# Kernel tuning notes

Hardware: AMD Instinct MI355X
Metric: run time of the kernel (lower is better)

## Reference

```python
import jax, jax.numpy as jnp
import numpy as np

D = 512; NH = 8; NL = 6; DFF = 2048
TOK = 1024; APP = 3; V = TOK + APP; PAD = V - 1
B = 256; SENC = 16; LTGT = 62


def setup_inputs() -> dict:
    key = jax.random.key(0)
    ks = jax.random.split(key, 14)
    g = lambda k, shp, s=0.02: jax.random.normal(k, shp, jnp.float32) * s
    return dict(
        encoder_out=jax.random.normal(ks[0], (B, SENC, D), jnp.float32),
        point_out=jax.random.normal(ks[1], (B, D), jnp.float32),
        emb=g(ks[2], (V, D)),
        pos_embed=g(ks[3], (1, LTGT, D)),
        sa_inw=g(ks[4], (NL, 3 * D, D)), sa_inb=jnp.zeros((NL, 3 * D), jnp.float32),
        sa_outw=g(ks[5], (NL, D, D)), sa_outb=jnp.zeros((NL, D), jnp.float32),
        ca_inw=g(ks[6], (NL, 3 * D, D)), ca_inb=jnp.zeros((NL, 3 * D), jnp.float32),
        ca_outw=g(ks[7], (NL, D, D)), ca_outb=jnp.zeros((NL, D), jnp.float32),
        ln1_s=jnp.ones((NL, D), jnp.float32), ln1_b=jnp.zeros((NL, D), jnp.float32),
        ln2_s=jnp.ones((NL, D), jnp.float32), ln2_b=jnp.zeros((NL, D), jnp.float32),
        ln3_s=jnp.ones((NL, D), jnp.float32), ln3_b=jnp.zeros((NL, D), jnp.float32),
        ff1_w=g(ks[8], (NL, DFF, D)), ff1_b=jnp.zeros((NL, DFF), jnp.float32),
        ff2_w=g(ks[9], (NL, D, DFF)), ff2_b=jnp.zeros((NL, D), jnp.float32),
        out_w=g(ks[10], (V, D)), out_b=jnp.zeros((V,), jnp.float32),
        tgt=jax.random.randint(ks[11], (B, LTGT), 0, TOK),
    )


def _ln(x, s, b, eps=1e-5):
    m = x.mean(-1, keepdims=True)
    v = ((x - m) ** 2).mean(-1, keepdims=True)
    return (x - m) / jnp.sqrt(v + eps) * s + b


def _mha(q_in, kv_in, inw, inb, outw, outb, mask):
    # PyTorch MultiheadAttention with packed in_proj [3D, D]
    hd = D // NH
    wq, wk, wv = inw[:D], inw[D:2 * D], inw[2 * D:]
    bq, bk, bv = inb[:D], inb[D:2 * D], inb[2 * D:]
    Bq, Tq = q_in.shape[0], q_in.shape[1]
    Tk = kv_in.shape[1]
    q = (q_in @ wq.T + bq).reshape(Bq, Tq, NH, hd)
    k = (kv_in @ wk.T + bk).reshape(Bq, Tk, NH, hd)
    v = (kv_in @ wv.T + bv).reshape(Bq, Tk, NH, hd)
    s = jnp.einsum('bqhd,bkhd->bhqk', q, k) / np.float32(np.sqrt(hd))
    if mask is not None:
        s = s + mask
    a = jax.nn.softmax(s, axis=-1)
    o = jnp.einsum('bhqk,bkhd->bqhd', a, v).reshape(Bq, Tq, D)
    return o @ outw.T + outb


def reference(encoder_out, point_out, emb, pos_embed,
              sa_inw, sa_inb, sa_outw, sa_outb,
              ca_inw, ca_inb, ca_outw, ca_outb,
              ln1_s, ln1_b, ln2_s, ln2_b, ln3_s, ln3_b,
              ff1_w, ff1_b, ff2_w, ff2_b, out_w, out_b, tgt):
    # scheduled_sampling_ratio == 1.0 => the per-step loop always writes the
    # ground-truth token, so output_sequence == tgt[:, :-1] and the returned
    # tensor equals one full causal decoder pass over tgt[:, :-1].
    tokens = tgt[:, :-1]                      # [B, L], L = 61
    L = tokens.shape[1]
    neg = jnp.float32(-jnp.inf)
    causal = jnp.where(jnp.triu(jnp.ones((L, L), bool), 1), neg, 0.0)
    padm = jnp.where(tokens == PAD, neg, 0.0)[:, None, None, :]  # [B,1,1,L]
    mask = causal[None, None] + padm          # [B,1,L,L]
    mem = encoder_out[:, :1, :]               # memory length 1 (encoder_out[:, [0]])
    x = emb[tokens] + point_out[:, None, :] + pos_embed[0, :L]
    for i in range(NL):
        x = _ln(x + _mha(x, x, sa_inw[i], sa_inb[i], sa_outw[i], sa_outb[i], mask), ln1_s[i], ln1_b[i])
        x = _ln(x + _mha(x, mem, ca_inw[i], ca_inb[i], ca_outw[i], ca_outb[i], None), ln2_s[i], ln2_b[i])
        h = jax.nn.relu(x @ ff1_w[i].T + ff1_b[i]) @ ff2_w[i].T + ff2_b[i]
        x = _ln(x + h, ln3_s[i], ln3_b[i])
    return x @ out_w.T + out_b               # [B, L, V]
```

## Files before the change

kernel.cpp:

```cpp
#include <hip/hip_runtime.h>
#include <stdint.h>
#include <stddef.h>

typedef unsigned short u16;
typedef float f4 __attribute__((ext_vector_type(4)));
typedef float f32x4 __attribute__((ext_vector_type(4)));
typedef short bf16x8 __attribute__((ext_vector_type(8)));
typedef u16 u16x4 __attribute__((ext_vector_type(4)));
typedef int i4v __attribute__((ext_vector_type(4)));

#define PAD_TOK 1026
#define LQ 61
#define NBATCH 256
#define MTOT (NBATCH * LQ)

__device__ __forceinline__ u16 f2b(float f) {
  uint32_t x = __float_as_uint(f);
  x += 0x7fff + ((x >> 16) & 1);
  return (u16)(x >> 16);
}
__device__ __forceinline__ float b2f(u16 u) {
  return __uint_as_float(((uint32_t)u) << 16);
}

template<int BM>
__global__ __launch_bounds__(256) void gemm_bt(
    const u16* __restrict__ A, const u16* __restrict__ W,
    const float* __restrict__ bias,
    float* __restrict__ Cf, u16* __restrict__ Cb,
    int M, int N, int K, int Nreal, int ldc, int relu,
    long aZ, long wZ, long bZ, long cZ)
{
  constexpr int MI = BM / 32;
  const int z = blockIdx.z;
  A += z * aZ; W += z * wZ; bias += z * bZ;
  if (Cf) Cf += z * cZ;
  if (Cb) Cb += z * cZ;

  __shared__ u16 As[BM * 64];
  __shared__ u16 Bs[128 * 64];

  const int gx = gridDim.x;
  const int nwg = gx * gridDim.y;
  const int orig = blockIdx.y * gx + blockIdx.x;
  const int q8 = nwg >> 3, r8 = nwg & 7;
  const int xcd = orig & 7, off = orig >> 3;
  const int nid = (xcd < r8 ? xcd * (q8 + 1) : r8 * (q8 + 1) + (xcd - r8) * q8) + off;
  const int bx = nid % gx, by = nid / gx;

  const int tid = threadIdx.x;
  const int wid = tid >> 6, lane = tid & 63;
  const int wr = wid >> 1, wc = wid & 1;
  const long m0 = (long)by * BM;
  const long n0 = (long)bx * 128;

  const int lr = lane >> 3;
  const int lc = lane & 7;
  const int scol = ((lc ^ lr) << 3);

  f32x4 acc[MI][4];
#pragma unroll
  for (int i = 0; i < MI; ++i)
#pragma unroll
    for (int j = 0; j < 4; ++j) acc[i][j] = (f32x4){0.f, 0.f, 0.f, 0.f};

  const u16* Abase = A + m0 * K;
  const u16* Wbase = W + n0 * K;
  const int r = lane & 15, kg = lane >> 4;

  for (int kt = 0; kt < K; kt += 64) {
#pragma unroll
    for (int c = 0; c < BM / 32; ++c) {
      const int row = wid * (BM / 4) + c * 8;
      __builtin_amdgcn_global_load_lds(
          (const __attribute__((address_space(1))) void*)(Abase + (long)(row + lr) * K + kt + scol),
          (__attribute__((address_space(3))) void*)&As[row * 64], 16, 0, 0);
    }
#pragma unroll
    for (int c = 0; c < 4; ++c) {
      const int row = wid * 32 + c * 8;
      __builtin_amdgcn_global_load_lds(
          (const __attribute__((address_space(1))) void*)(Wbase + (long)(row + lr) * K + kt + scol),
          (__attribute__((address_space(3))) void*)&Bs[row * 64], 16, 0, 0);
    }
    __syncthreads();

#pragma unroll
    for (int ks = 0; ks < 64; ks += 32) {
      bf16x8 a[MI], b[4];
#pragma unroll
      for (int mi = 0; mi < MI; ++mi) {
        const int row = wr * (BM / 2) + mi * 16 + r;
        const int chunk = ((ks >> 3) + kg) ^ (row & 7);
        a[mi] = *(const bf16x8*)&As[row * 64 + chunk * 8];
      }
#pragma unroll
      for (int ni = 0; ni < 4; ++ni) {
        const int row = wc * 64 + ni * 16 + r;
        const int chunk = ((ks >> 3) + kg) ^ (row & 7);
        b[ni] = *(const bf16x8*)&Bs[row * 64 + chunk * 8];
      }
#pragma unroll
      for (int mi = 0; mi < MI; ++mi)
#pragma unroll
        for (int ni = 0; ni < 4; ++ni)
          acc[mi][ni] = __builtin_amdgcn_mfma_f32_16x16x32_bf16(a[mi], b[ni], acc[mi][ni], 0, 0, 0);
    }
    __syncthreads();
  }

  const int cr4 = (lane >> 4) * 4;
  const int cc = lane & 15;

  if (Cb) {
#pragma unroll
    for (int ni = 0; ni < 4; ++ni) {
      const int coll = wc * 64 + ni * 16 + cc;
      const float bv = bias[(int)n0 + coll];
#pragma unroll
      for (int mi = 0; mi < MI; ++mi) {
#pragma unroll
        for (int j = 0; j < 4; ++j) {
          const int rowl = wr * (BM / 2) + mi * 16 + cr4 + j;
          float v = acc[mi][ni][j] + bv;
          if (relu) v = fmaxf(v, 0.f);
          const int sw = (rowl & 7) << 3;
          u16* half = (coll & 64) ? Bs : As;
          half[rowl * 64 + ((coll & 63) ^ sw)] = f2b(v);
        }
      }
    }
    __syncthreads();
    constexpr int PT = BM / 16;
#pragma unroll
    for (int i = 0; i < PT; ++i) {
      const int t = i * 256 + tid;
      const int row = t >> 4, ch = t & 15;
      const int n = (int)n0 + ch * 8;
      if (n < Nreal) {
        const int phys = (ch & 7) ^ (row & 7);
        const u16* half = (ch < 8) ? As : Bs;
        bf16x8 vv = *(const bf16x8*)&half[row * 64 + phys * 8];
        *(bf16x8*)&Cb[(m0 + row) * (long)N + n] = vv;
      }
    }
  } else {
#pragma unroll
    for (int ni = 0; ni < 4; ++ni) {
      const int n = (int)n0 + wc * 64 + ni * 16 + cc;
      if (n >= Nreal) continue;
      const float bv = bias[n];
#pragma unroll
      for (int mi = 0; mi < MI; ++mi) {
#pragma unroll
        for (int j = 0; j < 4; ++j) {
          const long m = m0 + wr * (BM / 2) + mi * 16 + cr4 + j;
          float v = acc[mi][ni][j] + bv;
          if (relu) v = fmaxf(v, 0.f);
          Cf[m * ldc + n] = v;
        }
      }
    }
  }
}

__global__ __launch_bounds__(256) void attn_k(const u16* __restrict__ qkv,
                                              const int* __restrict__ tgt,
                                              u16* __restrict__ outp)
{
  __shared__ u16 Qs[64 * 72];
  __shared__ u16 Ks[64 * 72];
  __shared__ u16 Vt[64 * 72];
  __shared__ float S[64 * 65];
  __shared__ int stok[64];

  const int bid = blockIdx.x;
  const int b = bid >> 3, h = bid & 7;
  const int tid = threadIdx.x;
  const int tr = tid >> 2, seg = tid & 3;

  if (tid < 64) stok[tid] = (tid < 61) ? tgt[b * 62 + tid] : -1;

  const long rowbase = ((long)(b * LQ + tr)) * 1536 + h * 64;
  if (tr < LQ) {
    const i4v* qsrc = (const i4v*)(qkv + rowbase + seg * 16);
    i4v q0 = qsrc[0], q1 = qsrc[1];
    *(i4v*)&Qs[tr * 72 + seg * 16] = q0;
    *(i4v*)&Qs[tr * 72 + seg * 16 + 8] = q1;
    const i4v* ksrc = (const i4v*)(qkv + rowbase + 512 + seg * 16);
    i4v k0 = ksrc[0], k1 = ksrc[1];
    *(i4v*)&Ks[tr * 72 + seg * 16] = k0;
    *(i4v*)&Ks[tr * 72 + seg * 16 + 8] = k1;
    const u16* vsrc = qkv + rowbase + 1024 + seg * 16;
#pragma unroll
    for (int i = 0; i < 16; ++i) Vt[(seg * 16 + i) * 72 + tr] = vsrc[i];
  } else {
    i4v zz = {0, 0, 0, 0};
    *(i4v*)&Qs[tr * 72 + seg * 16] = zz;
    *(i4v*)&Qs[tr * 72 + seg * 16 + 8] = zz;
    *(i4v*)&Ks[tr * 72 + seg * 16] = zz;
    *(i4v*)&Ks[tr * 72 + seg * 16 + 8] = zz;
#pragma unroll
    for (int i = 0; i < 16; ++i) Vt[(seg * 16 + i) * 72 + tr] = 0;
  }
  __syncthreads();

  const int lane = tid & 63, w = tid >> 6;
  const int r = lane & 15, kg = lane >> 4;

  {
    f32x4 s[4];
#pragma unroll
    for (int ni = 0; ni < 4; ++ni) s[ni] = (f32x4){0.f, 0.f, 0.f, 0.f};
    bf16x8 a0 = *(const bf16x8*)&Qs[(w * 16 + r) * 72 + kg * 8];
    bf16x8 a1 = *(const bf16x8*)&Qs[(w * 16 + r) * 72 + 32 + kg * 8];
#pragma unroll
    for (int ni = 0; ni < 4; ++ni) {
      bf16x8 b0 = *(const bf16x8*)&Ks[(ni * 16 + r) * 72 + kg * 8];
      bf16x8 b1 = *(const bf16x8*)&Ks[(ni * 16 + r) * 72 + 32 + kg * 8];
      s[ni] = __builtin_amdgcn_mfma_f32_16x16x32_bf16(a0, b0, s[ni], 0, 0, 0);
      s[ni] = __builtin_amdgcn_mfma_f32_16x16x32_bf16(a1, b1, s[ni], 0, 0, 0);
    }
#pragma unroll
    for (int ni = 0; ni < 4; ++ni)
#pragma unroll
      for (int j = 0; j < 4; ++j)
        S[(w * 16 + kg * 4 + j) * 65 + ni * 16 + r] = s[ni][j];
  }
  __syncthreads();

  {
    const int row = tid >> 2, g = tid & 3;
    float vals[16];
    float mx = -3e38f;
#pragma unroll
    for (int i = 0; i < 16; ++i) {
      const int k = g * 16 + i;
      float v = S[row * 65 + k] * 0.125f;
      const bool ok = (k <= row) && (k < LQ) && (stok[k] != PAD_TOK);
      v = ok ? v : -1e30f;
      vals[i] = v;
      mx = fmaxf(mx, v);
    }
    mx = fmaxf(mx, __shfl_xor(mx, 1));
    mx = fmaxf(mx, __shfl_xor(mx, 2));
    float sum = 0.f;
#pragma unroll
    for (int i = 0; i < 16; ++i) { float e = __expf(vals[i] - mx); vals[i] = e; sum += e; }
    sum += __shfl_xor(sum, 1);
    sum += __shfl_xor(sum, 2);
    const float inv = 1.f / sum;
#pragma unroll
    for (int i = 0; i < 16; ++i) Qs[row * 72 + g * 16 + i] = f2b(vals[i] * inv);
  }
  __syncthreads();

  {
    f32x4 o[4];
#pragma unroll
    for (int ni = 0; ni < 4; ++ni) o[ni] = (f32x4){0.f, 0.f, 0.f, 0.f};
    bf16x8 a0 = *(const bf16x8*)&Qs[(w * 16 + r) * 72 + kg * 8];
    bf16x8 a1 = *(const bf16x8*)&Qs[(w * 16 + r) * 72 + 32 + kg * 8];
#pragma unroll
    for (int ni = 0; ni < 4; ++ni) {
      bf16x8 b0 = *(const bf16x8*)&Vt[(ni * 16 + r) * 72 + kg * 8];
      bf16x8 b1 = *(const bf16x8*)&Vt[(ni * 16 + r) * 72 + 32 + kg * 8];
      o[ni] = __builtin_amdgcn_mfma_f32_16x16x32_bf16(a0, b0, o[ni], 0, 0, 0);
      o[ni] = __builtin_amdgcn_mfma_f32_16x16x32_bf16(a1, b1, o[ni], 0, 0, 0);
    }
#pragma unroll
    for (int ni = 0; ni < 4; ++ni)
#pragma unroll
      for (int j = 0; j < 4; ++j) {
        const int qrow = w * 16 + kg * 4 + j;
        const int col = ni * 16 + r;
        Ks[qrow * 64 + (col ^ ((qrow & 7) << 3))] = f2b(o[ni][j]);
      }
  }
  __syncthreads();

  {
    const int row = tid >> 2, sub = tid & 3;
    if (row < LQ) {
      const long obase = ((long)(b * LQ + row)) * 512 + h * 64;
#pragma unroll
      for (int i = 0; i < 2; ++i) {
        const int ch = i * 4 + sub;
        const int phys = ch ^ (row & 7);
        bf16x8 vv = *(const bf16x8*)&Ks[row * 64 + phys * 8];
        *(bf16x8*)&outp[obase + ch * 8] = vv;
      }
    }
  }
}

__device__ __forceinline__ void ln_row(f4& v0, f4& v1,
                                       const float* __restrict__ sw,
                                       const float* __restrict__ bw, int d0) {
  float s1 = v0[0] + v0[1] + v0[2] + v0[3] + v1[0] + v1[1] + v1[2] + v1[3];
  float s2 = v0[0]*v0[0] + v0[1]*v0[1] + v0[2]*v0[2] + v0[3]*v0[3]
           + v1[0]*v1[0] + v1[1]*v1[1] + v1[2]*v1[2] + v1[3]*v1[3];
#pragma unroll
  for (int off = 1; off < 64; off <<= 1) {
    s1 += __shfl_xor(s1, off);
    s2 += __shfl_xor(s2, off);
  }
  const float mean = s1 * (1.f / 512.f);
  const float var = s2 * (1.f / 512.f) - mean * mean;
  const float rstd = rsqrtf(var + 1e-5f);
  const f4* sp = (const f4*)(sw + d0);
  const f4* bp = (const f4*)(bw + d0);
  f4 ss0 = sp[0], ss1 = sp[1], bb0 = bp[0], bb1 = bp[1];
#pragma unroll
  for (int i = 0; i < 4; ++i) {
    v0[i] = (v0[i] - mean) * rstd * ss0[i] + bb0[i];
    v1[i] = (v1[i] - mean) * rstd * ss1[i] + bb1[i];
  }
}

template<bool CA>
__global__ __launch_bounds__(256) void lnf_k(const u16* __restrict__ p,
                                             const u16* __restrict__ xr,
                                             const float* __restrict__ cav,
                                             const float* __restrict__ s1,
                                             const float* __restrict__ b1,
                                             const float* __restrict__ s2,
                                             const float* __restrict__ b2,
                                             u16* __restrict__ out)
{
  const int m = blockIdx.x * 4 + (threadIdx.x >> 6);
  const int lane = threadIdx.x & 63;
  const int d0 = lane * 8;
  bf16x8 pv = *(const bf16x8*)(p + (long)m * 512 + d0);
  bf16x8 xv = *(const bf16x8*)(xr + (long)m * 512 + d0);
  f4 v0, v1;
#pragma unroll
  for (int i = 0; i < 4; ++i) {
    v0[i] = b2f((u16)pv[i]) + b2f((u16)xv[i]);
    v1[i] = b2f((u16)pv[4 + i]) + b2f((u16)xv[4 + i]);
  }
  ln_row(v0, v1, s1, b1, d0);
  if constexpr (CA) {
    const int b = m / LQ;
    const f4* qv = (const f4*)(cav + (long)b * 512 + d0);
    v0 += qv[0]; v1 += qv[1];
    ln_row(v0, v1, s2, b2, d0);
  }
  u16x4* ob = (u16x4*)(out + (long)m * 512 + d0);
  ob[0] = (u16x4){f2b(v0[0]), f2b(v0[1]), f2b(v0[2]), f2b(v0[3])};
  ob[1] = (u16x4){f2b(v1[0]), f2b(v1[1]), f2b(v1[2]), f2b(v1[3])};
}

__global__ __launch_bounds__(256) void embed_k(const float* __restrict__ emb,
                                               const float* __restrict__ pout,
                                               const float* __restrict__ pos,
                                               const int* __restrict__ tgt,
                                               u16* __restrict__ XB)
{
  const int m = blockIdx.x * 4 + (threadIdx.x >> 6);
  const int lane = threadIdx.x & 63;
  const int b = m / LQ, t = m % LQ;
  const int tok = tgt[b * 62 + t];
  const int d0 = lane * 8;
  const f4* e = (const f4*)(emb + (long)tok * 512 + d0);
  const f4* p = (const f4*)(pout + (long)b * 512 + d0);
  const f4* q = (const f4*)(pos + (long)t * 512 + d0);
  f4 v0 = e[0] + p[0] + q[0];
  f4 v1 = e[1] + p[1] + q[1];
  u16x4* xb = (u16x4*)(XB + (long)m * 512 + d0);
  xb[0] = (u16x4){f2b(v0[0]), f2b(v0[1]), f2b(v0[2]), f2b(v0[3])};
  xb[1] = (u16x4){f2b(v1[0]), f2b(v1[1]), f2b(v1[2]), f2b(v1[3])};
}

__global__ void cvt_bf16_k(const float* __restrict__ src, u16* __restrict__ dst, int n4) {
  const int i = blockIdx.x * 256 + threadIdx.x;
  if (i >= n4) return;
  f4 v = ((const f4*)src)[i];
  ((u16x4*)dst)[i] = (u16x4){f2b(v[0]), f2b(v[1]), f2b(v[2]), f2b(v[3])};
}

__global__ void cvt_ca_v_k(const float* __restrict__ ca_inw, u16* __restrict__ dst) {
  const int i = blockIdx.x * 256 + threadIdx.x;
  if (i >= 393216) return;
  const int l = i >> 16, rem = i & 65535;
  f4 v = ((const f4*)ca_inw)[l * 196608 + 131072 + rem];
  ((u16x4*)dst)[i] = (u16x4){f2b(v[0]), f2b(v[1]), f2b(v[2]), f2b(v[3])};
}

__global__ void cvt_outw_k(const float* __restrict__ out_w, u16* __restrict__ dst) {
  const int i = blockIdx.x * 256 + threadIdx.x;
  if (i >= 147456) return;
  const int row = (i * 4) >> 9;
  u16x4 o = {0, 0, 0, 0};
  if (row < 1027) {
    f4 v = ((const f4*)out_w)[i];
    o = (u16x4){f2b(v[0]), f2b(v[1]), f2b(v[2]), f2b(v[3])};
  }
  ((u16x4*)dst)[i] = o;
}

__global__ void cvt_outb_k(const float* __restrict__ out_b, float* __restrict__ dst) {
  const int i = blockIdx.x * 256 + threadIdx.x;
  if (i >= 1152) return;
  dst[i] = (i < 1027) ? out_b[i] : 0.f;
}

__global__ void cvt_memb_k(const float* __restrict__ enc, u16* __restrict__ dst) {
  const int i = blockIdx.x * 256 + threadIdx.x;
  if (i >= 32768) return;
  const int b = (i * 4) >> 9, d = (i * 4) & 511;
  f4 v = ((const f4*)enc)[(b * 8192 + d) >> 2];
  ((u16x4*)dst)[i] = (u16x4){f2b(v[0]), f2b(v[1]), f2b(v[2]), f2b(v[3])};
}

static constexpr size_t XB_OFF    = 0;
static constexpr size_t P_OFF     = 15990784;
static constexpr size_t BIG_OFF   = 31981568;
static constexpr size_t ATT_OFF   = 95944704;
static constexpr size_t WSA_OFF   = 111935488;
static constexpr size_t WSO_OFF   = 121372672;
static constexpr size_t WCAV_OFF  = 124518400;
static constexpr size_t WCO_OFF   = 127664128;
static constexpr size_t WF1_OFF   = 130809856;
static constexpr size_t WF2_OFF   = 143392768;
static constexpr size_t WOUT_OFF  = 155975680;
static constexpr size_t BOUT_OFF  = 157155328;
static constexpr size_t MEMB_OFF  = 157159936;
static constexpr size_t CATMP_OFF = 157422080;
static constexpr size_t CAV_OFF   = 158994944;

extern "C" void kernel_launch(void* const* d_in, const int* in_sizes, int n_in,
                              void* d_out, int out_size, void* d_ws, size_t ws_size,
                              hipStream_t stream) {
  (void)in_sizes; (void)n_in; (void)out_size; (void)ws_size;
  const float* encoder_out = (const float*)d_in[0];
  const float* point_out   = (const float*)d_in[1];
  const float* emb         = (const float*)d_in[2];
  const float* pos         = (const float*)d_in[3];
  const float* sa_inw      = (const float*)d_in[4];
  const float* sa_inb      = (const float*)d_in[5];
  const float* sa_outw     = (const float*)d_in[6];
  const float* sa_outb     = (const float*)d_in[7];
  const float* ca_inw      = (const float*)d_in[8];
  const float* ca_inb      = (const float*)d_in[9];
  const float* ca_outw     = (const float*)d_in[10];
  const float* ca_outb     = (const float*)d_in[11];
  const float* ln1_s       = (const float*)d_in[12];
  const float* ln1_b       = (const float*)d_in[13];
  const float* ln2_s       = (const float*)d_in[14];
  const float* ln2_b       = (const float*)d_in[15];
  const float* ln3_s       = (const float*)d_in[16];
  const float* ln3_b       = (const float*)d_in[17];
  const float* ff1_w       = (const float*)d_in[18];
  const float* ff1_b       = (const float*)d_in[19];
  const float* ff2_w       = (const float*)d_in[20];
  const float* ff2_b       = (const float*)d_in[21];
  const float* out_w       = (const float*)d_in[22];
  const float* out_b       = (const float*)d_in[23];
  const int*   tgt         = (const int*)d_in[24];

  char* ws = (char*)d_ws;
  u16*   XB    = (u16*)(ws + XB_OFF);
  u16*   P     = (u16*)(ws + P_OFF);
  u16*   BIG   = (u16*)(ws + BIG_OFF);
  u16*   ATT   = (u16*)(ws + ATT_OFF);
  u16*   WSA   = (u16*)(ws + WSA_OFF);
  u16*   WSO   = (u16*)(ws + WSO_OFF);
  u16*   WCAV  = (u16*)(ws + WCAV_OFF);
  u16*   WCO   = (u16*)(ws + WCO_OFF);
  u16*   WF1   = (u16*)(ws + WF1_OFF);
  u16*   WF2   = (u16*)(ws + WF2_OFF);
  u16*   WOUT  = (u16*)(ws + WOUT_OFF);
  float* BOUT  = (float*)(ws + BOUT_OFF);
  u16*   MEMB  = (u16*)(ws + MEMB_OFF);
  u16*   CATMP = (u16*)(ws + CATMP_OFF);
  float* CAV   = (float*)(ws + CAV_OFF);

  cvt_bf16_k<<<dim3(4608), dim3(256), 0, stream>>>(sa_inw, WSA, 1179648);
  cvt_bf16_k<<<dim3(1536), dim3(256), 0, stream>>>(sa_outw, WSO, 393216);
  cvt_ca_v_k<<<dim3(1536), dim3(256), 0, stream>>>(ca_inw, WCAV);
  cvt_bf16_k<<<dim3(1536), dim3(256), 0, stream>>>(ca_outw, WCO, 393216);
  cvt_bf16_k<<<dim3(6144), dim3(256), 0, stream>>>(ff1_w, WF1, 1572864);
  cvt_bf16_k<<<dim3(6144), dim3(256), 0, stream>>>(ff2_w, WF2, 1572864);
  cvt_outw_k<<<dim3(576), dim3(256), 0, stream>>>(out_w, WOUT);
  cvt_outb_k<<<dim3(5), dim3(256), 0, stream>>>(out_b, BOUT);
  cvt_memb_k<<<dim3(128), dim3(256), 0, stream>>>(encoder_out, MEMB);

  embed_k<<<dim3(MTOT / 4), dim3(256), 0, stream>>>(emb, point_out, pos, tgt, XB);

  gemm_bt<64><<<dim3(4, 4, 6), dim3(256), 0, stream>>>(
      MEMB, WCAV, ca_inb + 1024, nullptr, CATMP,
      256, 512, 512, 512, 512, 0,
      0L, 262144L, 1536L, 131072L);
  gemm_bt<64><<<dim3(4, 4, 6), dim3(256), 0, stream>>>(
      CATMP, WCO, ca_outb, CAV, nullptr,
      256, 512, 512, 512, 512, 0,
      131072L, 262144L, 512L, 131072L);

  for (int l = 0; l < 6; ++l) {
    gemm_bt<128><<<dim3(12, 122, 1), dim3(256), 0, stream>>>(
        XB, WSA + (long)l * 786432, sa_inb + l * 1536, nullptr, BIG,
        MTOT, 1536, 512, 1536, 1536, 0, 0L, 0L, 0L, 0L);
    attn_k<<<dim3(2048), dim3(256), 0, stream>>>(BIG, tgt, ATT);
    gemm_bt<64><<<dim3(4, 244, 1), dim3(256), 0, stream>>>(
        ATT, WSO + (long)l * 262144, sa_outb + l * 512, nullptr, P,
        MTOT, 512, 512, 512, 512, 0, 0L, 0L, 0L, 0L);
    lnf_k<true><<<dim3(MTOT / 4), dim3(256), 0, stream>>>(
        P, XB, CAV + (long)l * 131072,
        ln1_s + l * 512, ln1_b + l * 512, ln2_s + l * 512, ln2_b + l * 512, XB);
    gemm_bt<128><<<dim3(16, 122, 1), dim3(256), 0, stream>>>(
        XB, WF1 + (long)l * 1048576, ff1_b + l * 2048, nullptr, BIG,
        MTOT, 2048, 512, 2048, 2048, 1, 0L, 0L, 0L, 0L);
    gemm_bt<64><<<dim3(4, 244, 1), dim3(256), 0, stream>>>(
        BIG, WF2 + (long)l * 1048576, ff2_b + l * 512, nullptr, P,
        MTOT, 512, 2048, 512, 512, 0, 0L, 0L, 0L, 0L);
    lnf_k<false><<<dim3(MTOT / 4), dim3(256), 0, stream>>>(
        P, XB, nullptr, ln3_s + l * 512, ln3_b + l * 512, nullptr, nullptr, XB);
  }

  gemm_bt<128><<<dim3(9, 122, 1), dim3(256), 0, stream>>>(
      XB, WOUT, BOUT, (float*)d_out, nullptr,
      MTOT, 1152, 512, 1027, 1027, 0, 0L, 0L, 0L, 0L);
}
```

Baseline: 1.216 ms.

## Add 256x256-tile 8-wave GEMM with direct-to-LDS loads for QKV, FF1, output

After: 1.187 ms. 2.4% less time.

```diff
diff --git a/kernel.cpp b/kernel.cpp
--- a/kernel.cpp
+++ b/kernel.cpp
@@ -21,6 +21,203 @@
 }
 __device__ __forceinline__ float b2f(u16 u) {
   return __uint_as_float(((uint32_t)u) << 16);
+}
+
+#define GLDS(gptr, lptr) __builtin_amdgcn_global_load_lds( \
+    (const __attribute__((address_space(1))) void*)(gptr), \
+    (__attribute__((address_space(3))) void*)(lptr), 16, 0, 0)
+
+__device__ __forceinline__ bf16x8 ldfrag(const u16* buf, int row, int ksl, int kg) {
+  const int chunk = (ksl * 4 + kg) ^ (row & 7);
+  return *(const bf16x8*)&buf[row * 64 + chunk * 8];
+}
+
+__global__ __launch_bounds__(512, 2) void gemm8_k(
+    const u16* __restrict__ A, const u16* __restrict__ W,
+    const float* __restrict__ bias,
+    float* __restrict__ Cf, u16* __restrict__ Cb,
+    int N, int K, int Nreal, int ldc, int relu)
+{
+  __shared__ u16 lds[4][16384];
+  u16* const LA0 = lds[0];
+  u16* const LB0 = lds[1];
+  u16* const LA1 = lds[2];
+  u16* const LB1 = lds[3];
+
+  const int gx = gridDim.x;
+  const int nwg = gx * gridDim.y;
+  const int orig = blockIdx.y * gx + blockIdx.x;
+  const int q8 = nwg >> 3, r8 = nwg & 7;
+  const int xcd = orig & 7, off = orig >> 3;
+  const int nid = (xcd < r8 ? xcd * (q8 + 1) : r8 * (q8 + 1) + (xcd - r8) * q8) + off;
+  const int bx = nid % gx, by = nid / gx;
+
+  const int tid = threadIdx.x;
+  const int wid = tid >> 6, lane = tid & 63;
+  const int wm = wid >> 2, wn = wid & 3;
+  const long m0 = (long)by * 256;
+  const long n0 = (long)bx * 256;
+
+  const int lr = lane >> 3, lc = lane & 7;
+  const int scol = ((lc ^ lr) << 3);
+  const int r = lane & 15, kg = lane >> 4;
+
+  const u16* __restrict__ Ab = A + m0 * K;
+  const u16* __restrict__ Wb = W + n0 * K;
+
+  f32x4 acc[8][4];
+#pragma unroll
+  for (int i = 0; i < 8; ++i)
+#pragma unroll
+    for (int j = 0; j < 4; ++j) acc[i][j] = (f32x4){0.f, 0.f, 0.f, 0.f};
+
+#define ST64(gbase, kt, ldsbuf, r0) do {                                     \
+    const int rb_ = (r0) + wid * 8;                                          \
+    GLDS((gbase) + (long)(rb_ + lr) * K + (kt) + scol, &(ldsbuf)[rb_ * 64]); \
+  } while (0)
+#define STAQ(kt, ldsbuf, q_) do {                                            \
+    const int rb_ = ((wid & 4) ? 128 : 0) + (q_) * 32 + (wid & 3) * 8;       \
+    GLDS(Ab + (long)(rb_ + lr) * K + (kt) + scol, &(ldsbuf)[rb_ * 64]);      \
+  } while (0)
+#define STB(kt, ldsbuf) do {            \
+    ST64(Wb, kt, ldsbuf, 0);   ST64(Wb, kt, ldsbuf, 64);  \
+    ST64(Wb, kt, ldsbuf, 128); ST64(Wb, kt, ldsbuf, 192); \
+  } while (0)
+#define STAF(kt, ldsbuf) do {           \
+    ST64(Ab, kt, ldsbuf, 0);   ST64(Ab, kt, ldsbuf, 64);  \
+    ST64(Ab, kt, ldsbuf, 128); ST64(Ab, kt, ldsbuf, 192); \
+  } while (0)
+#define ENDBAR do { __builtin_amdgcn_sched_barrier(0); __builtin_amdgcn_s_barrier(); } while (0)
+#define PHASE(bufA, q_) do {                                                 \
+    bf16x8 a_[2][2];                                                         \
+    _Pragma("unroll")                                                        \
+    for (int ml = 0; ml < 2; ++ml)                                           \
+      _Pragma("unroll")                                                      \
+      for (int ks = 0; ks < 2; ++ks)                                         \
+        a_[ml][ks] = ldfrag(bufA, wm * 128 + ((q_) * 2 + ml) * 16 + r, ks, kg); \
+    __builtin_amdgcn_s_setprio(1);                                           \
+    _Pragma("unroll")                                                        \
+    for (int ml = 0; ml < 2; ++ml)                                           \
+      _Pragma("unroll")                                                      \
+      for (int ni = 0; ni < 4; ++ni) {                                       \
+        acc[(q_) * 2 + ml][ni] = __builtin_amdgcn_mfma_f32_16x16x32_bf16(    \
+            a_[ml][0], bf[ni][0], acc[(q_) * 2 + ml][ni], 0, 0, 0);          \
+        acc[(q_) * 2 + ml][ni] = __builtin_amdgcn_mfma_f32_16x16x32_bf16(    \
+            a_[ml][1], bf[ni][1], acc[(q_) * 2 + ml][ni], 0, 0, 0);          \
+      }                                                                      \
+    __builtin_amdgcn_s_setprio(0);                                           \
+  } while (0)
+
+  STAF(0, LA0); STB(0, LB0);
+  STAF(64, LA1); STB(64, LB1);
+
+  const int nits = K >> 7;
+  bf16x8 bf[4][2];
+
+  for (int it = 0; it < nits; ++it) {
+    const int kt1 = it * 128 + 64;
+    const int ktA = it * 128 + 128;
+    const int ktB = it * 128 + 192;
+    const bool last = (it == nits - 1);
+
+    asm volatile("s_waitcnt vmcnt(7)" ::: "memory");
+    ENDBAR;
+    if (it > 0) STAQ(kt1, LA1, 3);
+#pragma unroll
+    for (int ni = 0; ni < 4; ++ni)
+#pragma unroll
+      for (int ks = 0; ks < 2; ++ks)
+        bf[ni][ks] = ldfrag(LB0, wn * 64 + ni * 16 + r, ks, kg);
+    PHASE(LA0, 0);
+    ENDBAR;
+    if (!last) { STAQ(ktA, LA0, 0); STB(ktA, LB0); }
+    PHASE(LA0, 1);
+    ENDBAR;
+    if (!last) STAQ(ktA, LA0, 1);
+    PHASE(LA0, 2);
+    ENDBAR;
+    if (!last) STAQ(ktA, LA0, 2);
+    PHASE(LA0, 3);
+    ENDBAR;
+    if (last) asm volatile("s_waitcnt vmcnt(0)" ::: "memory");
+    else      asm volatile("s_waitcnt vmcnt(7)" ::: "memory");
+    ENDBAR;
+    if (!last) STAQ(ktA, LA0, 3);
+#pragma unroll
+    for (int ni = 0; ni < 4; ++ni)
+#pragma unroll
+      for (int ks = 0; ks < 2; ++ks)
+        bf[ni][ks] = ldfrag(LB1, wn * 64 + ni * 16 + r, ks, kg);
+    PHASE(LA1, 0);
+    ENDBAR;
+    if (!last) { STAQ(ktB, LA1, 0); STB(ktB, LB1); }
+    PHASE(LA1, 1);
+    ENDBAR;
+    if (!last) STAQ(ktB, LA1, 1);
+    PHASE(LA1, 2);
+    ENDBAR;
+    if (!last) STAQ(ktB, LA1, 2);
+    PHASE(LA1, 3);
+    ENDBAR;
+  }
+
+  const int cr4 = (lane >> 4) * 4;
+  const int cc = lane & 15;
+  if (Cb) {
+    u16* cbuf = &lds[0][0];
+#pragma unroll
+    for (int ni = 0; ni < 4; ++ni) {
+      const int coll = wn * 64 + ni * 16 + cc;
+      const float bv = bias[(int)n0 + coll];
+#pragma unroll
+      for (int mi = 0; mi < 8; ++mi) {
+#pragma unroll
+        for (int j = 0; j < 4; ++j) {
+          const int rowl = wm * 128 + mi * 16 + cr4 + j;
+          float v = acc[mi][ni][j] + bv;
+          if (relu) v = fmaxf(v, 0.f);
+          const int ch = coll >> 3;
+          const int phys = ch ^ (rowl & 31);
+          cbuf[rowl * 256 + phys * 8 + (coll & 7)] = f2b(v);
+        }
+      }
+    }
+    ENDBAR;
+#pragma unroll
+    for (int i = 0; i < 16; ++i) {
+      const int t = i * 512 + tid;
+      const int row = t >> 5, ch = t & 31;
+      const int n = (int)n0 + ch * 8;
+      if (n < Nreal) {
+        const int phys = ch ^ (row & 31);
+        *(bf16x8*)&Cb[(m0 + row) * (long)N + n] =
+            *(const bf16x8*)&cbuf[row * 256 + phys * 8];
+      }
+    }
+  } else {
+#pragma unroll
+    for (int ni = 0; ni < 4; ++ni) {
+      const int n = (int)n0 + wn * 64 + ni * 16 + cc;
+      if (n >= Nreal) continue;
+      const float bv = bias[n];
+#pragma unroll
+      for (int mi = 0; mi < 8; ++mi) {
+#pragma unroll
+        for (int j = 0; j < 4; ++j) {
+          const long m = m0 + wm * 128 + mi * 16 + cr4 + j;
+          float v = acc[mi][ni][j] + bv;
+          if (relu) v = fmaxf(v, 0.f);
+          Cf[m * ldc + n] = v;
+        }
+      }
+    }
+  }
+#undef ST64
+#undef STAQ
+#undef STB
+#undef STAF
+#undef ENDBAR
+#undef PHASE
 }
 
 template<int BM>
@@ -389,7 +586,7 @@
 
 __global__ void cvt_outw_k(const float* __restrict__ out_w, u16* __restrict__ dst) {
   const int i = blockIdx.x * 256 + threadIdx.x;
-  if (i >= 147456) return;
+  if (i >= 163840) return;
   const int row = (i * 4) >> 9;
   u16x4 o = {0, 0, 0, 0};
   if (row < 1027) {
@@ -401,7 +598,7 @@
 
 __global__ void cvt_outb_k(const float* __restrict__ out_b, float* __restrict__ dst) {
   const int i = blockIdx.x * 256 + threadIdx.x;
-  if (i >= 1152) return;
+  if (i >= 1280) return;
   dst[i] = (i < 1027) ? out_b[i] : 0.f;
 }
 
@@ -424,10 +621,10 @@
 static constexpr size_t WF1_OFF   = 130809856;
 static constexpr size_t WF2_OFF   = 143392768;
 static constexpr size_t WOUT_OFF  = 155975680;
-static constexpr size_t BOUT_OFF  = 157155328;
-static constexpr size_t MEMB_OFF  = 157159936;
-static constexpr size_t CATMP_OFF = 157422080;
-static constexpr size_t CAV_OFF   = 158994944;
+static constexpr size_t BOUT_OFF  = 157286400;
+static constexpr size_t MEMB_OFF  = 157291520;
+static constexpr size_t CATMP_OFF = 157553664;
+static constexpr size_t CAV_OFF   = 159126528;
 
 extern "C" void kernel_launch(void* const* d_in, const int* in_sizes, int n_in,
                               void* d_out, int out_size, void* d_ws, size_t ws_size,
@@ -482,7 +679,7 @@
   cvt_bf16_k<<<dim3(1536), dim3(256), 0, stream>>>(ca_outw, WCO, 393216);
   cvt_bf16_k<<<dim3(6144), dim3(256), 0, stream>>>(ff1_w, WF1, 1572864);
   cvt_bf16_k<<<dim3(6144), dim3(256), 0, stream>>>(ff2_w, WF2, 1572864);
-  cvt_outw_k<<<dim3(576), dim3(256), 0, stream>>>(out_w, WOUT);
+  cvt_outw_k<<<dim3(640), dim3(256), 0, stream>>>(out_w, WOUT);
   cvt_outb_k<<<dim3(5), dim3(256), 0, stream>>>(out_b, BOUT);
   cvt_memb_k<<<dim3(128), dim3(256), 0, stream>>>(encoder_out, MEMB);
 
@@ -498,9 +695,9 @@
       131072L, 262144L, 512L, 131072L);
 
   for (int l = 0; l < 6; ++l) {
-    gemm_bt<128><<<dim3(12, 122, 1), dim3(256), 0, stream>>>(
+    gemm8_k<<<dim3(6, 61), dim3(512), 0, stream>>>(
         XB, WSA + (long)l * 786432, sa_inb + l * 1536, nullptr, BIG,
-        MTOT, 1536, 512, 1536, 1536, 0, 0L, 0L, 0L, 0L);
+        1536, 512, 1536, 1536, 0);
     attn_k<<<dim3(2048), dim3(256), 0, stream>>>(BIG, tgt, ATT);
     gemm_bt<64><<<dim3(4, 244, 1), dim3(256), 0, stream>>>(
         ATT, WSO + (long)l * 262144, sa_outb + l * 512, nullptr, P,
@@ -508,9 +705,9 @@
     lnf_k<true><<<dim3(MTOT / 4), dim3(256), 0, stream>>>(
         P, XB, CAV + (long)l * 131072,
         ln1_s + l * 512, ln1_b + l * 512, ln2_s + l * 512, ln2_b + l * 512, XB);
-    gemm_bt<128><<<dim3(16, 122, 1), dim3(256), 0, stream>>>(
+    gemm8_k<<<dim3(8, 61), dim3(512), 0, stream>>>(
         XB, WF1 + (long)l * 1048576, ff1_b + l * 2048, nullptr, BIG,
-        MTOT, 2048, 512, 2048, 2048, 1, 0L, 0L, 0L, 0L);
+        2048, 512, 2048, 2048, 1);
     gemm_bt<64><<<dim3(4, 244, 1), dim3(256), 0, stream>>>(
         BIG, WF2 + (long)l * 1048576, ff2_b + l * 512, nullptr, P,
         MTOT, 512, 2048, 512, 512, 0, 0L, 0L, 0L, 0L);
@@ -518,7 +715,7 @@
         P, XB, nullptr, ln3_s + l * 512, ln3_b + l * 512, nullptr, nullptr, XB);
   }
 
-  gemm_bt<128><<<dim3(9, 122, 1), dim3(256), 0, stream>>>(
+  gemm8_k<<<dim3(5, 61), dim3(512), 0, stream>>>(
       XB, WOUT, BOUT, (float*)d_out, nullptr,
-      MTOT, 1152, 512, 1027, 1027, 0, 0L, 0L, 0L, 0L);
-}
+      1280, 512, 1027, 1027, 0);
+}
```

## Fuse output-projection and FFN2 GEMMs with residual add and LayerNorm epilogue

Applied to the files above, without the earlier changes.

New measurement: 1.303 ms. 7.1% more time.

```diff
diff --git a/kernel.cpp b/kernel.cpp
--- a/kernel.cpp
+++ b/kernel.cpp
@@ -21,6 +21,15 @@
 }
 __device__ __forceinline__ float b2f(u16 u) {
   return __uint_as_float(((uint32_t)u) << 16);
+}
+
+#define GLDS(gptr, lptr) __builtin_amdgcn_global_load_lds( \
+    (const __attribute__((address_space(1))) void*)(gptr), \
+    (__attribute__((address_space(3))) void*)(lptr), 16, 0, 0)
+
+__device__ __forceinline__ bf16x8 ldfrag(const u16* buf, int row, int ksl, int kg) {
+  const int chunk = (ksl * 4 + kg) ^ (row & 7);
+  return *(const bf16x8*)&buf[row * 64 + chunk * 8];
 }
 
 template<int BM>
@@ -72,34 +81,24 @@
 #pragma unroll
     for (int c = 0; c < BM / 32; ++c) {
       const int row = wid * (BM / 4) + c * 8;
-      __builtin_amdgcn_global_load_lds(
-          (const __attribute__((address_space(1))) void*)(Abase + (long)(row + lr) * K + kt + scol),
-          (__attribute__((address_space(3))) void*)&As[row * 64], 16, 0, 0);
+      GLDS(Abase + (long)(row + lr) * K + kt + scol, &As[row * 64]);
     }
 #pragma unroll
     for (int c = 0; c < 4; ++c) {
       const int row = wid * 32 + c * 8;
-      __builtin_amdgcn_global_load_lds(
-          (const __attribute__((address_space(1))) void*)(Wbase + (long)(row + lr) * K + kt + scol),
-          (__attribute__((address_space(3))) void*)&Bs[row * 64], 16, 0, 0);
+      GLDS(Wbase + (long)(row + lr) * K + kt + scol, &Bs[row * 64]);
     }
     __syncthreads();
 
 #pragma unroll
-    for (int ks = 0; ks < 64; ks += 32) {
+    for (int ks = 0; ks < 2; ++ks) {
       bf16x8 a[MI], b[4];
 #pragma unroll
-      for (int mi = 0; mi < MI; ++mi) {
-        const int row = wr * (BM / 2) + mi * 16 + r;
-        const int chunk = ((ks >> 3) + kg) ^ (row & 7);
-        a[mi] = *(const bf16x8*)&As[row * 64 + chunk * 8];
-      }
-#pragma unroll
-      for (int ni = 0; ni < 4; ++ni) {
-        const int row = wc * 64 + ni * 16 + r;
-        const int chunk = ((ks >> 3) + kg) ^ (row & 7);
-        b[ni] = *(const bf16x8*)&Bs[row * 64 + chunk * 8];
-      }
+      for (int mi = 0; mi < MI; ++mi)
+        a[mi] = ldfrag(As, wr * (BM / 2) + mi * 16 + r, ks, kg);
+#pragma unroll
+      for (int ni = 0; ni < 4; ++ni)
+        b[ni] = ldfrag(Bs, wc * 64 + ni * 16 + r, ks, kg);
 #pragma unroll
       for (int mi = 0; mi < MI; ++mi)
 #pragma unroll
@@ -161,6 +160,229 @@
         }
       }
     }
+  }
+}
+
+template<bool CA2>
+__global__ __launch_bounds__(512, 2) void gemmln_k(
+    const u16* __restrict__ A, const u16* __restrict__ W,
+    const float* __restrict__ bias,
+    const u16* __restrict__ cavb,
+    const float* __restrict__ s1w, const float* __restrict__ b1w,
+    const float* __restrict__ s2w, const float* __restrict__ b2w,
+    u16* __restrict__ XB, int K)
+{
+  __shared__ u16 BIGL[36864];
+  __shared__ float LSTAT[64][8];
+  __shared__ u16 LCAV[1536];
+  u16* const LB = BIGL;
+  u16* const LA = BIGL + 32768;
+  u16* const EP = BIGL;
+
+  const int nwg = gridDim.x;
+  const int orig = blockIdx.x;
+  const int q8 = nwg >> 3, r8 = nwg & 7;
+  const int xcd = orig & 7, off = orig >> 3;
+  const int by = (xcd < r8 ? xcd * (q8 + 1) : r8 * (q8 + 1) + (xcd - r8) * q8) + off;
+
+  const int tid = threadIdx.x;
+  const int wid = tid >> 6, lane = tid & 63;
+  const int wm = wid >> 2, wn = wid & 3;
+  const long m0 = (long)by * 64;
+
+  const int lr = lane >> 3, lc = lane & 7;
+  const int scol = ((lc ^ lr) << 3);
+  const int r = lane & 15, kg = lane >> 4;
+
+  f32x4 acc[2][8];
+#pragma unroll
+  for (int i = 0; i < 2; ++i)
+#pragma unroll
+    for (int j = 0; j < 8; ++j) acc[i][j] = (f32x4){0.f, 0.f, 0.f, 0.f};
+
+  const u16* Abase = A + m0 * K;
+
+  for (int kt = 0; kt < K; kt += 64) {
+    {
+      const int arow = wid * 8;
+      GLDS(Abase + (long)(arow + lr) * K + kt + scol, &LA[arow * 64]);
+#pragma unroll
+      for (int c = 0; c < 8; ++c) {
+        const int row = wid * 64 + c * 8;
+        GLDS(W + (long)(row + lr) * K + kt + scol, &LB[row * 64]);
+      }
+    }
+    __syncthreads();
+#pragma unroll
+    for (int ks = 0; ks < 2; ++ks) {
+      bf16x8 a0 = ldfrag(LA, wm * 32 + r, ks, kg);
+      bf16x8 a1 = ldfrag(LA, wm * 32 + 16 + r, ks, kg);
+#pragma unroll
+      for (int ni = 0; ni < 8; ++ni) {
+        bf16x8 b = ldfrag(LB, wn * 128 + ni * 16 + r, ks, kg);
+        acc[0][ni] = __builtin_amdgcn_mfma_f32_16x16x32_bf16(a0, b, acc[0][ni], 0, 0, 0);
+        acc[1][ni] = __builtin_amdgcn_mfma_f32_16x16x32_bf16(a1, b, acc[1][ni], 0, 0, 0);
+      }
+    }
+    __syncthreads();
+  }
+
+  const int b0 = (int)(m0 / LQ);
+  const int bsplit1 = (b0 + 1) * LQ;
+  const int bsplit2 = (b0 + 2) * LQ;
+
+#pragma unroll
+  for (int i = 0; i < 8; ++i) {
+    const int t = i * 512 + tid;
+    const int row = t >> 6, ch = t & 63;
+    *(bf16x8*)&EP[row * 516 + ch * 8] =
+        *(const bf16x8*)&XB[(m0 + row) * 512 + ch * 8];
+  }
+  if constexpr (CA2) {
+    for (int t = tid; t < 1536; t += 512) {
+      const int bb = t >> 9, c = t & 511;
+      int bi = b0 + bb;
+      if (bi > NBATCH - 1) bi = NBATCH - 1;
+      LCAV[bb * 512 + c] = cavb[(long)bi * 512 + c];
+    }
+  }
+  __syncthreads();
+
+  float bcol[8];
+#pragma unroll
+  for (int ni = 0; ni < 8; ++ni) bcol[ni] = bias[wn * 128 + ni * 16 + r];
+#pragma unroll
+  for (int mi = 0; mi < 2; ++mi)
+#pragma unroll
+    for (int ni = 0; ni < 8; ++ni) {
+      const int col = wn * 128 + ni * 16 + r;
+#pragma unroll
+      for (int j = 0; j < 4; ++j) {
+        const int row = wm * 32 + mi * 16 + kg * 4 + j;
+        acc[mi][ni][j] += bcol[ni] + b2f(EP[row * 516 + col]);
+      }
+    }
+
+#pragma unroll
+  for (int mi = 0; mi < 2; ++mi)
+#pragma unroll
+    for (int j = 0; j < 4; ++j) {
+      float s1 = 0.f, s2 = 0.f;
+#pragma unroll
+      for (int ni = 0; ni < 8; ++ni) {
+        const float v = acc[mi][ni][j];
+        s1 += v; s2 += v * v;
+      }
+#pragma unroll
+      for (int o = 1; o < 16; o <<= 1) {
+        s1 += __shfl_xor(s1, o);
+        s2 += __shfl_xor(s2, o);
+      }
+      if (r == 0) {
+        const int row = wm * 32 + mi * 16 + kg * 4 + j;
+        LSTAT[row][wn] = s1;
+        LSTAT[row][4 + wn] = s2;
+      }
+    }
+  __syncthreads();
+
+  float sc[8], bc[8];
+#pragma unroll
+  for (int ni = 0; ni < 8; ++ni) {
+    const int col = wn * 128 + ni * 16 + r;
+    sc[ni] = s1w[col]; bc[ni] = b1w[col];
+  }
+#pragma unroll
+  for (int mi = 0; mi < 2; ++mi)
+#pragma unroll
+    for (int j = 0; j < 4; ++j) {
+      const int row = wm * 32 + mi * 16 + kg * 4 + j;
+      const float S1 = LSTAT[row][0] + LSTAT[row][1] + LSTAT[row][2] + LSTAT[row][3];
+      const float S2 = LSTAT[row][4] + LSTAT[row][5] + LSTAT[row][6] + LSTAT[row][7];
+      const float mean = S1 * (1.f / 512.f);
+      const float var = S2 * (1.f / 512.f) - mean * mean;
+      const float rstd = rsqrtf(var + 1e-5f);
+#pragma unroll
+      for (int ni = 0; ni < 8; ++ni)
+        acc[mi][ni][j] = (acc[mi][ni][j] - mean) * rstd * sc[ni] + bc[ni];
+    }
+
+  if constexpr (CA2) {
+#pragma unroll
+    for (int mi = 0; mi < 2; ++mi)
+#pragma unroll
+      for (int j = 0; j < 4; ++j) {
+        const int row = wm * 32 + mi * 16 + kg * 4 + j;
+        const int gr = (int)m0 + row;
+        const int sel = (gr >= bsplit2) ? 2 : ((gr >= bsplit1) ? 1 : 0);
+#pragma unroll
+        for (int ni = 0; ni < 8; ++ni) {
+          const int col = wn * 128 + ni * 16 + r;
+          acc[mi][ni][j] += b2f(LCAV[sel * 512 + col]);
+        }
+      }
+    __syncthreads();
+#pragma unroll
+    for (int mi = 0; mi < 2; ++mi)
+#pragma unroll
+      for (int j = 0; j < 4; ++j) {
+        float s1 = 0.f, s2 = 0.f;
+#pragma unroll
+        for (int ni = 0; ni < 8; ++ni) {
+          const float v = acc[mi][ni][j];
+          s1 += v; s2 += v * v;
+        }
+#pragma unroll
+        for (int o = 1; o < 16; o <<= 1) {
+          s1 += __shfl_xor(s1, o);
+          s2 += __shfl_xor(s2, o);
+        }
+        if (r == 0) {
+          const int row = wm * 32 + mi * 16 + kg * 4 + j;
+          LSTAT[row][wn] = s1;
+          LSTAT[row][4 + wn] = s2;
+        }
+      }
+    __syncthreads();
+#pragma unroll
+    for (int ni = 0; ni < 8; ++ni) {
+      const int col = wn * 128 + ni * 16 + r;
+      sc[ni] = s2w[col]; bc[ni] = b2w[col];
+    }
+#pragma unroll
+    for (int mi = 0; mi < 2; ++mi)
+#pragma unroll
+      for (int j = 0; j < 4; ++j) {
+        const int row = wm * 32 + mi * 16 + kg * 4 + j;
+        const float S1 = LSTAT[row][0] + LSTAT[row][1] + LSTAT[row][2] + LSTAT[row][3];
+        const float S2 = LSTAT[row][4] + LSTAT[row][5] + LSTAT[row][6] + LSTAT[row][7];
+        const float mean = S1 * (1.f / 512.f);
+        const float var = S2 * (1.f / 512.f) - mean * mean;
+        const float rstd = rsqrtf(var + 1e-5f);
+#pragma unroll
+        for (int ni = 0; ni < 8; ++ni)
+          acc[mi][ni][j] = (acc[mi][ni][j] - mean) * rstd * sc[ni] + bc[ni];
+      }
+  }
+
+#pragma unroll
+  for (int mi = 0; mi < 2; ++mi)
+#pragma unroll
+    for (int ni = 0; ni < 8; ++ni) {
+      const int col = wn * 128 + ni * 16 + r;
+#pragma unroll
+      for (int j = 0; j < 4; ++j) {
+        const int row = wm * 32 + mi * 16 + kg * 4 + j;
+        EP[row * 516 + col] = f2b(acc[mi][ni][j]);
+      }
+    }
+  __syncthreads();
+#pragma unroll
+  for (int i = 0; i < 8; ++i) {
+    const int t = i * 512 + tid;
+    const int row = t >> 6, ch = t & 63;
+    *(bf16x8*)&XB[(m0 + row) * 512 + ch * 8] =
+        *(const bf16x8*)&EP[row * 516 + ch * 8];
   }
 }
 
@@ -292,63 +514,6 @@
       }
     }
   }
-}
-
-__device__ __forceinline__ void ln_row(f4& v0, f4& v1,
-                                       const float* __restrict__ sw,
-                                       const float* __restrict__ bw, int d0) {
-  float s1 = v0[0] + v0[1] + v0[2] + v0[3] + v1[0] + v1[1] + v1[2] + v1[3];
-  float s2 = v0[0]*v0[0] + v0[1]*v0[1] + v0[2]*v0[2] + v0[3]*v0[3]
-           + v1[0]*v1[0] + v1[1]*v1[1] + v1[2]*v1[2] + v1[3]*v1[3];
-#pragma unroll
-  for (int off = 1; off < 64; off <<= 1) {
-    s1 += __shfl_xor(s1, off);
-    s2 += __shfl_xor(s2, off);
-  }
-  const float mean = s1 * (1.f / 512.f);
-  const float var = s2 * (1.f / 512.f) - mean * mean;
-  const float rstd = rsqrtf(var + 1e-5f);
-  const f4* sp = (const f4*)(sw + d0);
-  const f4* bp = (const f4*)(bw + d0);
-  f4 ss0 = sp[0], ss1 = sp[1], bb0 = bp[0], bb1 = bp[1];
-#pragma unroll
-  for (int i = 0; i < 4; ++i) {
-    v0[i] = (v0[i] - mean) * rstd * ss0[i] + bb0[i];
-    v1[i] = (v1[i] - mean) * rstd * ss1[i] + bb1[i];
-  }
-}
-
-template<bool CA>
-__global__ __launch_bounds__(256) void lnf_k(const u16* __restrict__ p,
-                                             const u16* __restrict__ xr,
-                                             const float* __restrict__ cav,
-                                             const float* __restrict__ s1,
-                                             const float* __restrict__ b1,
-                                             const float* __restrict__ s2,
-                                             const float* __restrict__ b2,
-                                             u16* __restrict__ out)
-{
-  const int m = blockIdx.x * 4 + (threadIdx.x >> 6);
-  const int lane = threadIdx.x & 63;
-  const int d0 = lane * 8;
-  bf16x8 pv = *(const bf16x8*)(p + (long)m * 512 + d0);
-  bf16x8 xv = *(const bf16x8*)(xr + (long)m * 512 + d0);
-  f4 v0, v1;
-#pragma unroll
-  for (int i = 0; i < 4; ++i) {
-    v0[i] = b2f((u16)pv[i]) + b2f((u16)xv[i]);
-    v1[i] = b2f((u16)pv[4 + i]) + b2f((u16)xv[4 + i]);
-  }
-  ln_row(v0, v1, s1, b1, d0);
-  if constexpr (CA) {
-    const int b = m / LQ;
-    const f4* qv = (const f4*)(cav + (long)b * 512 + d0);
-    v0 += qv[0]; v1 += qv[1];
-    ln_row(v0, v1, s2, b2, d0);
-  }
-  u16x4* ob = (u16x4*)(out + (long)m * 512 + d0);
-  ob[0] = (u16x4){f2b(v0[0]), f2b(v0[1]), f2b(v0[2]), f2b(v0[3])};
-  ob[1] = (u16x4){f2b(v1[0]), f2b(v1[1]), f2b(v1[2]), f2b(v1[3])};
 }
 
 __global__ __launch_bounds__(256) void embed_k(const float* __restrict__ emb,
@@ -372,11 +537,28 @@
   xb[1] = (u16x4){f2b(v1[0]), f2b(v1[1]), f2b(v1[2]), f2b(v1[3])};
 }
 
-__global__ void cvt_bf16_k(const float* __restrict__ src, u16* __restrict__ dst, int n4) {
-  const int i = blockIdx.x * 256 + threadIdx.x;
-  if (i >= n4) return;
-  f4 v = ((const f4*)src)[i];
-  ((u16x4*)dst)[i] = (u16x4){f2b(v[0]), f2b(v[1]), f2b(v[2]), f2b(v[3])};
+__global__ void cvtall_k(const float* __restrict__ s0, const float* __restrict__ s1,
+                         const float* __restrict__ s2, const float* __restrict__ s3,
+                         const float* __restrict__ s4,
+                         u16* __restrict__ d0, u16* __restrict__ d1,
+                         u16* __restrict__ d2, u16* __restrict__ d3,
+                         u16* __restrict__ d4)
+{
+  const int N0 = 1179648;
+  const int N1 = N0 + 393216;
+  const int N2 = N1 + 393216;
+  const int N3 = N2 + 1572864;
+  const int N4 = N3 + 1572864;
+  for (int i = blockIdx.x * 256 + threadIdx.x; i < N4; i += gridDim.x * 256) {
+    const float* s; u16* d; int k;
+    if (i < N0)      { s = s0; d = d0; k = i; }
+    else if (i < N1) { s = s1; d = d1; k = i - N0; }
+    else if (i < N2) { s = s2; d = d2; k = i - N1; }
+    else if (i < N3) { s = s3; d = d3; k = i - N2; }
+    else             { s = s4; d = d4; k = i - N3; }
+    f4 v = ((const f4*)s)[k];
+    ((u16x4*)d)[k] = (u16x4){f2b(v[0]), f2b(v[1]), f2b(v[2]), f2b(v[3])};
+  }
 }
 
 __global__ void cvt_ca_v_k(const float* __restrict__ ca_inw, u16* __restrict__ dst) {
@@ -414,20 +596,19 @@
 }
 
 static constexpr size_t XB_OFF    = 0;
-static constexpr size_t P_OFF     = 15990784;
-static constexpr size_t BIG_OFF   = 31981568;
-static constexpr size_t ATT_OFF   = 95944704;
-static constexpr size_t WSA_OFF   = 111935488;
-static constexpr size_t WSO_OFF   = 121372672;
-static constexpr size_t WCAV_OFF  = 124518400;
-static constexpr size_t WCO_OFF   = 127664128;
-static constexpr size_t WF1_OFF   = 130809856;
-static constexpr size_t WF2_OFF   = 143392768;
-static constexpr size_t WOUT_OFF  = 155975680;
-static constexpr size_t BOUT_OFF  = 157155328;
-static constexpr size_t MEMB_OFF  = 157159936;
-static constexpr size_t CATMP_OFF = 157422080;
-static constexpr size_t CAV_OFF   = 158994944;
+static constexpr size_t BIG_OFF   = 15990784;
+static constexpr size_t ATT_OFF   = 79953920;
+static constexpr size_t WSA_OFF   = 95944704;
+static constexpr size_t WSO_OFF   = 105381888;
+static constexpr size_t WCAV_OFF  = 108527616;
+static constexpr size_t WCO_OFF   = 111673344;
+static constexpr size_t WF1_OFF   = 114819072;
+static constexpr size_t WF2_OFF   = 127401984;
+static constexpr size_t WOUT_OFF  = 139984896;
+static constexpr size_t BOUT_OFF  = 141164544;
+static constexpr size_t MEMB_OFF  = 141169152;
+static constexpr size_t CATMP_OFF = 141431296;
+static constexpr size_t CAVB_OFF  = 143004160;
 
 extern "C" void kernel_launch(void* const* d_in, const int* in_sizes, int n_in,
                               void* d_out, int out_size, void* d_ws, size_t ws_size,
@@ -461,7 +642,6 @@
 
   char* ws = (char*)d_ws;
   u16*   XB    = (u16*)(ws + XB_OFF);
-  u16*   P     = (u16*)(ws + P_OFF);
   u16*   BIG   = (u16*)(ws + BIG_OFF);
   u16*   ATT   = (u16*)(ws + ATT_OFF);
   u16*   WSA   = (u16*)(ws + WSA_OFF);
@@ -474,14 +654,11 @@
   float* BOUT  = (float*)(ws + BOUT_OFF);
   u16*   MEMB  = (u16*)(ws + MEMB_OFF);
   u16*   CATMP = (u16*)(ws + CATMP_OFF);
-  float* CAV   = (float*)(ws + CAV_OFF);
-
-  cvt_bf16_k<<<dim3(4608), dim3(256), 0, stream>>>(sa_inw, WSA, 1179648);
-  cvt_bf16_k<<<dim3(1536), dim3(256), 0, stream>>>(sa_outw, WSO, 393216);
+  u16*   CAVB  = (u16*)(ws + CAVB_OFF);
+
+  cvtall_k<<<dim3(2048), dim3(256), 0, stream>>>(
+      sa_inw, sa_outw, ca_outw, ff1_w, ff2_w, WSA, WSO, WCO, WF1, WF2);
   cvt_ca_v_k<<<dim3(1536), dim3(256), 0, stream>>>(ca_inw, WCAV);
-  cvt_bf16_k<<<dim3(1536), dim3(256), 0, stream>>>(ca_outw, WCO, 393216);
-  cvt_bf16_k<<<dim3(6144), dim3(256), 0, stream>>>(ff1_w, WF1, 1572864);
-  cvt_bf16_k<<<dim3(6144), dim3(256), 0, stream>>>(ff2_w, WF2, 1572864);
   cvt_outw_k<<<dim3(576), dim3(256), 0, stream>>>(out_w, WOUT);
   cvt_outb_k<<<dim3(5), dim3(256), 0, stream>>>(out_b, BOUT);
   cvt_memb_k<<<dim3(128), dim3(256), 0, stream>>>(encoder_out, MEMB);
@@ -493,7 +670,7 @@
       256, 512, 512, 512, 512, 0,
       0L, 262144L, 1536L, 131072L);
   gemm_bt<64><<<dim3(4, 4, 6), dim3(256), 0, stream>>>(
-      CATMP, WCO, ca_outb, CAV, nullptr,
+      CATMP, WCO, ca_outb, nullptr, CAVB,
       256, 512, 512, 512, 512, 0,
       131072L, 262144L, 512L, 131072L);
 
@@ -502,20 +679,19 @@
         XB, WSA + (long)l * 786432, sa_inb + l * 1536, nullptr, BIG,
         MTOT, 1536, 512, 1536, 1536, 0, 0L, 0L, 0L, 0L);
     attn_k<<<dim3(2048), dim3(256), 0, stream>>>(BIG, tgt, ATT);
-    gemm_bt<64><<<dim3(4, 244, 1), dim3(256), 0, stream>>>(
-        ATT, WSO + (long)l * 262144, sa_outb + l * 512, nullptr, P,
-        MTOT, 512, 512, 512, 512, 0, 0L, 0L, 0L, 0L);
-    lnf_k<true><<<dim3(MTOT / 4), dim3(256), 0, stream>>>(
-        P, XB, CAV + (long)l * 131072,
-        ln1_s + l * 512, ln1_b + l * 512, ln2_s + l * 512, ln2_b + l * 512, XB);
+    gemmln_k<true><<<dim3(244), dim3(512), 0, stream>>>(
+        ATT, WSO + (long)l * 262144, sa_outb + l * 512,
+        CAVB + (long)l * 131072,
+        ln1_s + l * 512, ln1_b + l * 512, ln2_s + l * 512, ln2_b + l * 512,
+        XB, 512);
     gemm_bt<128><<<dim3(16, 122, 1), dim3(256), 0, stream>>>(
         XB, WF1 + (long)l * 1048576, ff1_b + l * 2048, nullptr, BIG,
         MTOT, 2048, 512, 2048, 2048, 1, 0L, 0L, 0L, 0L);
-    gemm_bt<64><<<dim3(4, 244, 1), dim3(256), 0, stream>>>(
-        BIG, WF2 + (long)l * 1048576, ff2_b + l * 512, nullptr, P,
-        MTOT, 512, 2048, 512, 512, 0, 0L, 0L, 0L, 0L);
-    lnf_k<false><<<dim3(MTOT / 4), dim3(256), 0, stream>>>(
-        P, XB, nullptr, ln3_s + l * 512, ln3_b + l * 512, nullptr, nullptr, XB);
+    gemmln_k<false><<<dim3(244), dim3(512), 0, stream>>>(
+        BIG, WF2 + (long)l * 1048576, ff2_b + l * 512,
+        nullptr,
+        ln3_s + l * 512, ln3_b + l * 512, nullptr, nullptr,
+        XB, 2048);
   }
 
   gemm_bt<128><<<dim3(9, 122, 1), dim3(256), 0, stream>>>(
```
